# Optimization experiments

Measured on AMD Instinct MI355X. Metric: run time of the kernel, lower is better.

## Reference

```python
import jax, jax.numpy as jnp
import numpy as np

B, S, HID = 2, 2048, 2048
NH, HD = 16, 128            # num heads, head dim (HID = NH*HD)
ROT = 64                    # rotary_dim
MASK_VALUE = -10000.0


def _rotate_every_two(x):
    # x: [..., d] with d even; interleaved (-x2, x1)
    x1 = x[..., ::2]
    x2 = x[..., 1::2]
    return jnp.stack((-x2, x1), axis=-1).reshape(x.shape)


def _fixed_sincos(seq_len, dim):
    inv_freq = 1.0 / (10000.0 ** (jnp.arange(0, dim, 2, dtype=jnp.float32) / dim))
    t = jnp.arange(seq_len, dtype=jnp.float32)
    ang = t[:, None] * inv_freq[None, :]          # [S, dim/2]
    return jnp.sin(ang), jnp.cos(ang)


def _apply_rope(x, sin, cos):
    # x: [B, S, H, rot]; sin/cos: [S, rot/2] -> repeat_interleave(2) -> [S, rot]
    sin = jnp.repeat(sin, 2, axis=-1)[None, :, None, :]
    cos = jnp.repeat(cos, 2, axis=-1)[None, :, None, :]
    return x * cos + _rotate_every_two(x) * sin


def setup_inputs() -> dict:
    key = jax.random.key(0)
    ks = jax.random.split(key, 7)
    w_scale = 1.0 / np.sqrt(HID)
    return {
        "hidden_states": jax.random.normal(ks[0], (B, S, HID), dtype=jnp.float32),
        "attention_mask": jnp.zeros((B, 1, 1, S), dtype=jnp.float32),
        "Wq": jax.random.normal(ks[1], (HID, HID), dtype=jnp.float32) * w_scale,
        "bq": jnp.zeros((HID,), dtype=jnp.float32),
        "Wk": jax.random.normal(ks[2], (HID, HID), dtype=jnp.float32) * w_scale,
        "bk": jnp.zeros((HID,), dtype=jnp.float32),
        "Wv": jax.random.normal(ks[3], (HID, HID), dtype=jnp.float32) * w_scale,
        "bv": jnp.zeros((HID,), dtype=jnp.float32),
    }


def reference(hidden_states, attention_mask, Wq, bq, Wk, bk, Wv, bv):
    # QKV projections (torch Linear: x @ W.T + b)
    q = (hidden_states @ Wq.T + bq).reshape(B, S, NH, HD)
    k = (hidden_states @ Wk.T + bk).reshape(B, S, NH, HD)
    v = (hidden_states @ Wv.T + bv).reshape(B, S, NH, HD)

    # Inline rotary on first ROT dims of q/k
    sin, cos = _fixed_sincos(S, ROT)
    q = jnp.concatenate([_apply_rope(q[..., :ROT], sin, cos), q[..., ROT:]], axis=-1)
    k = jnp.concatenate([_apply_rope(k[..., :ROT], sin, cos), k[..., ROT:]], axis=-1)

    # Scores [B, H, S, S]
    scores = jnp.einsum('bqhd,bkhd->bhqk', q, k) / np.sqrt(HD)

    # Causal mask + additive attention mask
    causal = jnp.tril(jnp.ones((S, S), dtype=bool))[None, None]
    scores = jnp.where(causal, scores, jnp.asarray(MASK_VALUE, scores.dtype))
    scores = scores + attention_mask

    probs = jax.nn.softmax(scores, axis=-1)
    ctx = jnp.einsum('bhqk,bkhd->bqhd', probs, v)
    return ctx.reshape(B, S, HID)
```

## Files before the change

### kernel.cpp

```cpp
#include <hip/hip_runtime.h>

typedef unsigned short bhalf;
typedef __attribute__((ext_vector_type(4))) float    f32x4;
typedef __attribute__((ext_vector_type(8))) short    s16x8;
typedef __attribute__((ext_vector_type(4))) float    floatx4;
typedef __attribute__((ext_vector_type(4))) unsigned int u32x4;
typedef __attribute__((ext_vector_type(4))) unsigned short u16x4;

#define B_  2
#define S_  2048
#define HID_ 2048
#define NH_ 16
#define HD_ 128
#define M_  (B_*S_)
#define MASKV (-10000.0f)

__device__ __forceinline__ bhalf f32_to_bf16(float f) {
    union { float f; unsigned int u; } v; v.f = f;
    unsigned int r = v.u + 0x7FFFu + ((v.u >> 16) & 1u);
    return (bhalf)(r >> 16);
}
__device__ __forceinline__ bhalf f32_to_bf16_trunc(float f) {
    union { float f; unsigned int u; } v; v.f = f;
    return (bhalf)(v.u >> 16);
}
__device__ __forceinline__ float bf16_to_f32(bhalf h) {
    union { unsigned int u; float f; } v; v.u = ((unsigned int)h) << 16;
    return v.f;
}

__device__ __forceinline__ void gl_lds16(const void* g, void* l) {
    __builtin_amdgcn_global_load_lds(
        (const __attribute__((address_space(1))) void*)g,
        (__attribute__((address_space(3))) void*)l, 16, 0, 0);
}

__global__ __launch_bounds__(256) void cast_all(const float* __restrict__ hs,
                                                const float* __restrict__ Wq,
                                                const float* __restrict__ Wk,
                                                const float* __restrict__ Wv,
                                                bhalf* __restrict__ dst) {
    int idx = blockIdx.x * 256 + threadIdx.x;
    const float* src;
    if (idx < 2097152)      src = hs + (size_t)idx * 4;
    else if (idx < 3145728) src = Wq + (size_t)(idx - 2097152) * 4;
    else if (idx < 4194304) src = Wk + (size_t)(idx - 3145728) * 4;
    else                    src = Wv + (size_t)(idx - 4194304) * 4;
    floatx4 f = *(const floatx4*)src;
    u16x4 o;
    o.x = f32_to_bf16(f.x); o.y = f32_to_bf16(f.y);
    o.z = f32_to_bf16(f.z); o.w = f32_to_bf16(f.w);
    *(u16x4*)(dst + (size_t)idx * 4) = o;
}

__global__ __launch_bounds__(256) void qkv_gemm(const bhalf* __restrict__ A,
                                                const bhalf* __restrict__ Wb,
                                                const float* __restrict__ bq,
                                                const float* __restrict__ bk,
                                                const float* __restrict__ bv,
                                                bhalf* __restrict__ Out,
                                                bhalf* __restrict__ VTo) {
    __shared__ __align__(16) bhalf As[128 * 32];
    __shared__ __align__(16) bhalf Bs[128 * 32];
    const int tid  = threadIdx.x;
    const int lane = tid & 63, w = tid >> 6;
    const int wy = w >> 1, wx = w & 1;
    const int quad = lane >> 4, l = lane & 15;
    const int m0 = blockIdx.x * 128, n0 = blockIdx.y * 128;
    const int z  = blockIdx.z;
    const bhalf* W    = Wb + (size_t)z * HID_ * HID_;
    const float* bias = (z == 0) ? bq : (z == 1) ? bk : bv;
    bhalf* out        = Out + (size_t)z * M_ * HID_;

    f32x4 acc[4][4] = {};

    for (int kt = 0; kt < HID_; kt += 32) {
#pragma unroll
        for (int j = 0; j < 2; ++j) {
            int slot0 = j * 256 + w * 64;
            int slot  = slot0 + lane;
            int row = slot >> 2;
            int cg  = (slot & 3) ^ ((row >> 1) & 3);
            gl_lds16(A + (size_t)(m0 + row) * HID_ + kt + cg * 8, As + slot0 * 8);
            gl_lds16(W + (size_t)(n0 + row) * HID_ + kt + cg * 8, Bs + slot0 * 8);
        }
        __syncthreads();
        s16x8 af[4], bfr[4];
#pragma unroll
        for (int mt = 0; mt < 4; ++mt) {
            int row = wy * 64 + mt * 16 + l;
            int cgs = quad ^ ((row >> 1) & 3);
            af[mt] = *(const s16x8*)(As + (row * 4 + cgs) * 8);
        }
#pragma unroll
        for (int nt = 0; nt < 4; ++nt) {
            int row = wx * 64 + nt * 16 + l;
            int cgs = quad ^ ((row >> 1) & 3);
            bfr[nt] = *(const s16x8*)(Bs + (row * 4 + cgs) * 8);
        }
#pragma unroll
        for (int mt = 0; mt < 4; ++mt)
#pragma unroll
            for (int nt = 0; nt < 4; ++nt)
                acc[mt][nt] = __builtin_amdgcn_mfma_f32_16x16x32_bf16(
                    af[mt], bfr[nt], acc[mt][nt], 0, 0, 0);
        __syncthreads();
    }
    if (z == 2) {
#pragma unroll
        for (int mt = 0; mt < 4; ++mt) {
#pragma unroll
            for (int nt = 0; nt < 4; ++nt) {
                int col = n0 + wx * 64 + nt * 16 + l;
                float bv_ = bias[col];
                int row0 = m0 + wy * 64 + mt * 16 + quad * 4;
                int bb = row0 >> 11, s0 = row0 & 2047;
                u16x4 o;
#pragma unroll
                for (int r = 0; r < 4; ++r) o[r] = f32_to_bf16(acc[mt][nt][r] + bv_);
                *(u16x4*)(VTo + ((size_t)(bb * 16) * 128 + col) * S_ + s0) = o;
            }
        }
    } else {
#pragma unroll
        for (int mt = 0; mt < 4; ++mt) {
#pragma unroll
            for (int nt = 0; nt < 4; ++nt) {
                int col = n0 + wx * 64 + nt * 16 + l;
                float bv_ = bias[col];
#pragma unroll
                for (int r = 0; r < 4; ++r) {
                    int row = m0 + wy * 64 + mt * 16 + quad * 4 + r;
                    out[(size_t)row * HID_ + col] = f32_to_bf16(acc[mt][nt][r] + bv_);
                }
            }
        }
    }
}

__global__ __launch_bounds__(256) void rope_table(float2* __restrict__ tab) {
    int idx = blockIdx.x * 256 + threadIdx.x;
    int i = idx & 31, s = idx >> 5;
    float inv = expf(-(float)i * 0.2878231366242557f);
    float ang = (float)s * inv;
    tab[idx] = make_float2(sinf(ang), cosf(ang));
}

__global__ __launch_bounds__(256) void rope_apply(bhalf* __restrict__ Qb,
                                                  bhalf* __restrict__ Kb,
                                                  const float2* __restrict__ tab) {
    int flat = blockIdx.x * 256 + threadIdx.x;
    int i = flat & 31;
    int h = (flat >> 5) & 15;
    int s = (flat >> 9) & 2047;
    int b = flat >> 20;
    size_t base = ((size_t)(b * S_ + s)) * HID_ + h * HD_ + 2 * i;
    float2 sc = tab[s * 32 + i];
    float c = sc.y, sn = sc.x;
    {
        unsigned int q = *(const unsigned int*)(Qb + base);
        float x0 = bf16_to_f32((bhalf)(q & 0xffff));
        float x1 = bf16_to_f32((bhalf)(q >> 16));
        unsigned int o = (unsigned int)f32_to_bf16(x0 * c - x1 * sn)
                       | ((unsigned int)f32_to_bf16(x1 * c + x0 * sn) << 16);
        *(unsigned int*)(Qb + base) = o;
    }
    {
        unsigned int k = *(const unsigned int*)(Kb + base);
        float x0 = bf16_to_f32((bhalf)(k & 0xffff));
        float x1 = bf16_to_f32((bhalf)(k >> 16));
        unsigned int o = (unsigned int)f32_to_bf16(x0 * c - x1 * sn)
                       | ((unsigned int)f32_to_bf16(x1 * c + x0 * sn) << 16);
        *(unsigned int*)(Kb + base) = o;
    }
}

__global__ __launch_bounds__(512, 2) void flash_attn(const bhalf* __restrict__ Qb,
                                                     const bhalf* __restrict__ Kb,
                                                     const bhalf* __restrict__ VT,
                                                     const float* __restrict__ amask,
                                                     float* __restrict__ out) {
    __shared__ __align__(16) bhalf Kbuf[2][2048 * 8];
    __shared__ __align__(16) bhalf Vbuf[2][2048 * 8];
    const int tid = threadIdx.x, lane = tid & 63, w = tid >> 6;
    const int quad = lane >> 4, l = lane & 15;
    const int qt = blockIdx.x, bh = blockIdx.y;
    const int b = bh >> 4, h = bh & 15;
    const bool is_hi = (w < 4);
    const int ws = w & 3;
    const int myrow = is_hi ? ((31 - qt) * 64 + ws * 16) : (qt * 64 + ws * 16);
    const int ch_hi   = (33 - qt) >> 1;
    const int lo_last = (qt * 64 + 63) >> 7;
    const int my_last = is_hi ? (ch_hi - 1) : lo_last;

    s16x8 qf[4];
    {
        const bhalf* Qrow = Qb + (size_t)(b * S_ + myrow + l) * HID_ + h * HD_;
#pragma unroll
        for (int ks = 0; ks < 4; ++ks)
            qf[ks] = *(const s16x8*)(Qrow + ks * 32 + quad * 8);
    }
    s16x8 ones;
#pragma unroll
    for (int j = 0; j < 8; ++j) ones[j] = (short)0x3F80;

    float m_run[4] = {-1e30f, -1e30f, -1e30f, -1e30f};
    f32x4 l_acc = {};
    f32x4 acc[8] = {};
    const int fpl = ((l >> 2) << 1) | (l & 1);

#pragma unroll
    for (int j = 0; j < 4; ++j) {
        int slot0 = j * 512 + w * 64;
        int slot  = slot0 + lane;
        int row = slot >> 4, x = slot & 15;
        int g   = (x & 8) | ((x ^ row) & 7);
        gl_lds16(Kb + (size_t)(b * S_ + row) * HID_ + h * HD_ + g * 8,
                 &Kbuf[0][slot0 * 8]);
        gl_lds16(VT + ((size_t)bh * HD_ + row) * S_ + g * 8,
                 &Vbuf[0][slot0 * 8]);
    }

    for (int kc = 0; kc < ch_hi; ++kc) {
        const int cur = kc & 1, nxt = cur ^ 1;
        const int key0 = kc * 128;
        __syncthreads();

        const bool active = (kc <= my_last);
        const bool diag   = (kc == my_last);

        float am[8];
        if (active) {
#pragma unroll
            for (int nt = 0; nt < 8; ++nt) am[nt] = amask[b * S_ + key0 + nt * 16 + l];
        }
        if (kc + 1 < ch_hi) {
            const int key1 = key0 + 128;
#pragma unroll
            for (int j = 0; j < 4; ++j) {
                int slot0 = j * 512 + w * 64;
                int slot  = slot0 + lane;
                int row = slot >> 4, x = slot & 15;
                int g   = (x & 8) | ((x ^ row) & 7);
                gl_lds16(Kb + (size_t)(b * S_ + key1 + row) * HID_ + h * HD_ + g * 8,
                         &Kbuf[nxt][slot0 * 8]);
                gl_lds16(VT + ((size_t)bh * HD_ + row) * S_ + key1 + g * 8,
                         &Vbuf[nxt][slot0 * 8]);
            }
        }

        const bhalf* Kc = &Kbuf[cur][0];
        const bhalf* Vc = &Vbuf[cur][0];
        bhalf* Pw = &Kbuf[cur][0] + w * 2048;

        f32x4 s[8] = {};
        if (active) {
#pragma unroll
            for (int nt = 0; nt < 8; ++nt) {
                int key = nt * 16 + l;
#pragma unroll
                for (int ks = 0; ks < 4; ++ks) {
                    int dg = ks * 4 + quad;
                    int x  = (dg & 8) | ((dg ^ key) & 7);
                    s16x8 kf = *(const s16x8*)(Kc + (key * 16 + x) * 8);
                    s[nt] = __builtin_amdgcn_mfma_f32_16x16x32_bf16(qf[ks], kf, s[nt], 0, 0, 0);
                }
            }
        }
        __asm__ __volatile__("s_waitcnt lgkmcnt(0)\n\ts_barrier" ::: "memory");

        if (active) {
#pragma unroll
            for (int r = 0; r < 4; ++r) {
                const int qrow = myrow + quad * 4 + r;
                float p[8];
#pragma unroll
                for (int nt = 0; nt < 8; ++nt) {
                    float v = s[nt][r] * 0.08838834764831845f;
                    if (diag) { int key = key0 + nt * 16 + l; v = (key > qrow) ? MASKV : v; }
                    p[nt] = v + am[nt];
                }
                float mx = fmaxf(fmaxf(fmaxf(p[0], p[1]), fmaxf(p[2], p[3])),
                                 fmaxf(fmaxf(p[4], p[5]), fmaxf(p[6], p[7])));
#pragma unroll
                for (int msk = 1; msk < 16; msk <<= 1) mx = fmaxf(mx, __shfl_xor(mx, msk, 64));
                float m_new = fmaxf(m_run[r], mx);
                float alpha = __expf(m_run[r] - m_new);
                m_run[r] = m_new;
                const int m  = quad * 4 + r;
                const int fm = (quad << 1) | (r & 1);
#pragma unroll
                for (int nt = 0; nt < 8; ++nt) {
                    float e = __expf(p[nt] - m_new);
                    int key = nt * 16 + l;
                    Pw[(m * 16 + ((key >> 3) ^ fm)) * 8 + (key & 7)] = f32_to_bf16_trunc(e);
                }
                l_acc[r] *= alpha;
#pragma unroll
                for (int nt = 0; nt < 8; ++nt) acc[nt][r] *= alpha;
            }
#pragma unroll
            for (int kstep = 0; kstep < 4; ++kstep) {
                int kg = kstep * 4 + quad;
                s16x8 pf = *(const s16x8*)(Pw + (l * 16 + (kg ^ fpl)) * 8);
                l_acc = __builtin_amdgcn_mfma_f32_16x16x32_bf16(pf, ones, l_acc, 0, 0, 0);
#pragma unroll
                for (int nt = 0; nt < 8; ++nt) {
                    int d = nt * 16 + l;
                    int x = (kg & 8) | ((kg ^ d) & 7);
                    s16x8 vf = *(const s16x8*)(Vc + (d * 16 + x) * 8);
                    acc[nt] = __builtin_amdgcn_mfma_f32_16x16x32_bf16(pf, vf, acc[nt], 0, 0, 0);
                }
            }
        }
    }

    float inv[4];
#pragma unroll
    for (int r = 0; r < 4; ++r) inv[r] = 1.f / l_acc[r];
#pragma unroll
    for (int nt = 0; nt < 8; ++nt) {
        int col = h * HD_ + nt * 16 + l;
#pragma unroll
        for (int r = 0; r < 4; ++r)
            out[(size_t)(b * S_ + myrow + quad * 4 + r) * HID_ + col] = acc[nt][r] * inv[r];
    }
}

extern "C" void kernel_launch(void* const* d_in, const int* in_sizes, int n_in,
                              void* d_out, int out_size, void* d_ws, size_t ws_size,
                              hipStream_t stream) {
    const float* hs    = (const float*)d_in[0];
    const float* amask = (const float*)d_in[1];
    const float* Wq    = (const float*)d_in[2];
    const float* bq    = (const float*)d_in[3];
    const float* Wk    = (const float*)d_in[4];
    const float* bk    = (const float*)d_in[5];
    const float* Wv    = (const float*)d_in[6];
    const float* bv    = (const float*)d_in[7];
    float* out = (float*)d_out;

    bhalf* hsb = (bhalf*)d_ws;
    bhalf* wqb = hsb + 8388608;
    bhalf* wkb = wqb + 4194304;
    bhalf* wvb = wkb + 4194304;
    bhalf* Qb  = wvb + 4194304;
    bhalf* Kb  = Qb + 8388608;
    bhalf* VTb = Kb + 8388608;
    float2* tab = (float2*)(VTb + 8388608);

    rope_table<<<256, 256, 0, stream>>>(tab);
    cast_all<<<20480, 256, 0, stream>>>(hs, Wq, Wk, Wv, hsb);
    qkv_gemm<<<dim3(32, 16, 3), 256, 0, stream>>>(hsb, wqb, bq, bk, bv, Qb, VTb);
    rope_apply<<<8192, 256, 0, stream>>>(Qb, Kb, tab);
    flash_attn<<<dim3(16, 32), 512, 0, stream>>>(Qb, Kb, VTb, amask, out);
}
```

Measured before the change: 374.8 us.

## Rewrite QKV GEMM with 256x256 tiles, double-buffered LDS and interleaved prefetch

The QKV projection GEMM moves from 128x128 tiles with single-buffered 32-wide K steps to 256x256 tiles on 512 threads, with 64-wide K steps and double-buffered LDS. Global-to-LDS loads for the next K tiles are issued in chunks between MFMA phases, with explicit vmcnt waits, barriers and setprio raised around the MFMA blocks. The aim is to increase data reuse per tile and hide memory latency behind matrix math. The cost is higher register and LDS use per block (128KB LDS, launch bounds of 2 blocks) and only 384 blocks in the grid, so GPU occupancy and fill may drop.

```diff
diff --git a/kernel.cpp b/kernel.cpp
--- a/kernel.cpp
+++ b/kernel.cpp
@@ -4,7 +4,6 @@
 typedef __attribute__((ext_vector_type(4))) float    f32x4;
 typedef __attribute__((ext_vector_type(8))) short    s16x8;
 typedef __attribute__((ext_vector_type(4))) float    floatx4;
-typedef __attribute__((ext_vector_type(4))) unsigned int u32x4;
 typedef __attribute__((ext_vector_type(4))) unsigned short u16x4;
 
 #define B_  2
@@ -33,6 +32,12 @@
     __builtin_amdgcn_global_load_lds(
         (const __attribute__((address_space(1))) void*)g,
         (__attribute__((address_space(3))) void*)l, 16, 0, 0);
+}
+
+__device__ __forceinline__ void pb() {
+    __builtin_amdgcn_sched_barrier(0);
+    __builtin_amdgcn_s_barrier();
+    __builtin_amdgcn_sched_barrier(0);
 }
 
 __global__ __launch_bounds__(256) void cast_all(const float* __restrict__ hs,
@@ -53,67 +58,142 @@
     *(u16x4*)(dst + (size_t)idx * 4) = o;
 }
 
-__global__ __launch_bounds__(256) void qkv_gemm(const bhalf* __restrict__ A,
-                                                const bhalf* __restrict__ Wb,
-                                                const float* __restrict__ bq,
-                                                const float* __restrict__ bk,
-                                                const float* __restrict__ bv,
-                                                bhalf* __restrict__ Out,
-                                                bhalf* __restrict__ VTo) {
-    __shared__ __align__(16) bhalf As[128 * 32];
-    __shared__ __align__(16) bhalf Bs[128 * 32];
+__global__ __launch_bounds__(512, 2) void qkv_gemm(const bhalf* __restrict__ A,
+                                                   const bhalf* __restrict__ Wb,
+                                                   const float* __restrict__ bq,
+                                                   const float* __restrict__ bk,
+                                                   const float* __restrict__ bv,
+                                                   bhalf* __restrict__ Out,
+                                                   bhalf* __restrict__ VTo) {
+    __shared__ __align__(16) bhalf As[2][16384];
+    __shared__ __align__(16) bhalf Bs[2][16384];
     const int tid  = threadIdx.x;
     const int lane = tid & 63, w = tid >> 6;
-    const int wy = w >> 1, wx = w & 1;
     const int quad = lane >> 4, l = lane & 15;
-    const int m0 = blockIdx.x * 128, n0 = blockIdx.y * 128;
+    const int wy = w >> 2, wx = w & 3;
+    const int m0 = blockIdx.x * 256, n0 = blockIdx.y * 256;
     const int z  = blockIdx.z;
     const bhalf* W    = Wb + (size_t)z * HID_ * HID_;
     const float* bias = (z == 0) ? bq : (z == 1) ? bk : bv;
     bhalf* out        = Out + (size_t)z * M_ * HID_;
 
-    f32x4 acc[4][4] = {};
-
-    for (int kt = 0; kt < HID_; kt += 32) {
-#pragma unroll
-        for (int j = 0; j < 2; ++j) {
-            int slot0 = j * 256 + w * 64;
-            int slot  = slot0 + lane;
-            int row = slot >> 2;
-            int cg  = (slot & 3) ^ ((row >> 1) & 3);
-            gl_lds16(A + (size_t)(m0 + row) * HID_ + kt + cg * 8, As + slot0 * 8);
-            gl_lds16(W + (size_t)(n0 + row) * HID_ + kt + cg * 8, Bs + slot0 * 8);
-        }
-        __syncthreads();
-        s16x8 af[4], bfr[4];
-#pragma unroll
-        for (int mt = 0; mt < 4; ++mt) {
-            int row = wy * 64 + mt * 16 + l;
-            int cgs = quad ^ ((row >> 1) & 3);
-            af[mt] = *(const s16x8*)(As + (row * 4 + cgs) * 8);
-        }
-#pragma unroll
-        for (int nt = 0; nt < 4; ++nt) {
-            int row = wx * 64 + nt * 16 + l;
-            int cgs = quad ^ ((row >> 1) & 3);
-            bfr[nt] = *(const s16x8*)(Bs + (row * 4 + cgs) * 8);
-        }
-#pragma unroll
-        for (int mt = 0; mt < 4; ++mt)
-#pragma unroll
-            for (int nt = 0; nt < 4; ++nt)
-                acc[mt][nt] = __builtin_amdgcn_mfma_f32_16x16x32_bf16(
-                    af[mt], bfr[nt], acc[mt][nt], 0, 0, 0);
-        __syncthreads();
-    }
+    const int row_s = tid >> 3;
+    const int kg_s  = (tid & 7) ^ (row_s & 7);
+
+#define SA(bf, t, u) gl_lds16(A + (size_t)(m0 + (u)*64 + row_s) * HID_ + (t)*64 + kg_s*8, \
+                              &As[bf][(u)*4096 + w*512])
+#define SB(bf, t, u) gl_lds16(W + (size_t)(n0 + (u)*64 + row_s) * HID_ + (t)*64 + kg_s*8, \
+                              &Bs[bf][(u)*4096 + w*512])
+#define FRAG(P, row, ks) (*(const s16x8*)((P) + (row)*64 + ((((ks)*4 + quad) ^ ((row)&7)) * 8)))
+
+    f32x4 acc[8][4] = {};
+
+    SA(0, 0, 0); SA(0, 0, 2);
+    SB(0, 0, 0); SB(0, 0, 1); SB(0, 0, 2); SB(0, 0, 3);
+    SA(0, 0, 1); SA(0, 0, 3);
+    SA(1, 1, 0); SA(1, 1, 2);
+    SB(1, 1, 0); SB(1, 1, 1); SB(1, 1, 2); SB(1, 1, 3);
+    asm volatile("s_waitcnt vmcnt(6)" ::: "memory");
+    pb();
+
+    for (int t = 0; t < 32; ++t) {
+        const int cur = t & 1, nxt = cur ^ 1;
+        const bhalf* Ac = &As[cur][0];
+        const bhalf* Bc = &Bs[cur][0];
+        const int arow = wy * 128 + l;
+        const int brow = wx * 64 + l;
+        s16x8 a[4][2], b01[2][2], b23[2][2];
+
+#pragma unroll
+        for (int mt = 0; mt < 4; ++mt)
+#pragma unroll
+            for (int ks = 0; ks < 2; ++ks)
+                a[mt][ks] = FRAG(Ac, arow + mt * 16, ks);
+#pragma unroll
+        for (int nt = 0; nt < 2; ++nt)
+#pragma unroll
+            for (int ks = 0; ks < 2; ++ks)
+                b01[nt][ks] = FRAG(Bc, brow + nt * 16, ks);
+        if (t + 1 < 32) { SA(nxt, t + 1, 1); SA(nxt, t + 1, 3); }
+        pb();
+        __builtin_amdgcn_s_setprio(1);
+#pragma unroll
+        for (int mt = 0; mt < 4; ++mt)
+#pragma unroll
+            for (int nt = 0; nt < 2; ++nt)
+#pragma unroll
+                for (int ks = 0; ks < 2; ++ks)
+                    acc[mt][nt] = __builtin_amdgcn_mfma_f32_16x16x32_bf16(
+                        a[mt][ks], b01[nt][ks], acc[mt][nt], 0, 0, 0);
+        __builtin_amdgcn_s_setprio(0);
+        pb();
+
+#pragma unroll
+        for (int nt = 0; nt < 2; ++nt)
+#pragma unroll
+            for (int ks = 0; ks < 2; ++ks)
+                b23[nt][ks] = FRAG(Bc, brow + (nt + 2) * 16, ks);
+        if (t + 2 < 32) { SA(cur, t + 2, 0); SA(cur, t + 2, 2); }
+        pb();
+        __builtin_amdgcn_s_setprio(1);
+#pragma unroll
+        for (int mt = 0; mt < 4; ++mt)
+#pragma unroll
+            for (int nt = 0; nt < 2; ++nt)
+#pragma unroll
+                for (int ks = 0; ks < 2; ++ks)
+                    acc[mt][nt + 2] = __builtin_amdgcn_mfma_f32_16x16x32_bf16(
+                        a[mt][ks], b23[nt][ks], acc[mt][nt + 2], 0, 0, 0);
+        __builtin_amdgcn_s_setprio(0);
+        pb();
+
+#pragma unroll
+        for (int mt = 0; mt < 4; ++mt)
+#pragma unroll
+            for (int ks = 0; ks < 2; ++ks)
+                a[mt][ks] = FRAG(Ac, arow + 64 + mt * 16, ks);
+        if (t + 2 < 32) { SB(cur, t + 2, 0); SB(cur, t + 2, 1); }
+        pb();
+        __builtin_amdgcn_s_setprio(1);
+#pragma unroll
+        for (int mt = 0; mt < 4; ++mt)
+#pragma unroll
+            for (int nt = 0; nt < 2; ++nt)
+#pragma unroll
+                for (int ks = 0; ks < 2; ++ks)
+                    acc[4 + mt][nt + 2] = __builtin_amdgcn_mfma_f32_16x16x32_bf16(
+                        a[mt][ks], b23[nt][ks], acc[4 + mt][nt + 2], 0, 0, 0);
+        __builtin_amdgcn_s_setprio(0);
+        pb();
+
+        if (t + 2 < 32) { SB(cur, t + 2, 2); SB(cur, t + 2, 3); }
+        if (t < 30) { asm volatile("s_waitcnt vmcnt(6)" ::: "memory"); }
+        else        { asm volatile("s_waitcnt vmcnt(0)" ::: "memory"); }
+        pb();
+        __builtin_amdgcn_s_setprio(1);
+#pragma unroll
+        for (int mt = 0; mt < 4; ++mt)
+#pragma unroll
+            for (int nt = 0; nt < 2; ++nt)
+#pragma unroll
+                for (int ks = 0; ks < 2; ++ks)
+                    acc[4 + mt][nt] = __builtin_amdgcn_mfma_f32_16x16x32_bf16(
+                        a[mt][ks], b01[nt][ks], acc[4 + mt][nt], 0, 0, 0);
+        __builtin_amdgcn_s_setprio(0);
+        pb();
+    }
+#undef SA
+#undef SB
+#undef FRAG
+
     if (z == 2) {
 #pragma unroll
-        for (int mt = 0; mt < 4; ++mt) {
+        for (int mt = 0; mt < 8; ++mt) {
 #pragma unroll
             for (int nt = 0; nt < 4; ++nt) {
                 int col = n0 + wx * 64 + nt * 16 + l;
                 float bv_ = bias[col];
-                int row0 = m0 + wy * 64 + mt * 16 + quad * 4;
+                int row0 = m0 + wy * 128 + mt * 16 + quad * 4;
                 int bb = row0 >> 11, s0 = row0 & 2047;
                 u16x4 o;
 #pragma unroll
@@ -123,14 +203,14 @@
         }
     } else {
 #pragma unroll
-        for (int mt = 0; mt < 4; ++mt) {
+        for (int mt = 0; mt < 8; ++mt) {
 #pragma unroll
             for (int nt = 0; nt < 4; ++nt) {
                 int col = n0 + wx * 64 + nt * 16 + l;
                 float bv_ = bias[col];
 #pragma unroll
                 for (int r = 0; r < 4; ++r) {
-                    int row = m0 + wy * 64 + mt * 16 + quad * 4 + r;
+                    int row = m0 + wy * 128 + mt * 16 + quad * 4 + r;
                     out[(size_t)row * HID_ + col] = f32_to_bf16(acc[mt][nt][r] + bv_);
                 }
             }
@@ -351,7 +431,7 @@
 
     rope_table<<<256, 256, 0, stream>>>(tab);
     cast_all<<<20480, 256, 0, stream>>>(hs, Wq, Wk, Wv, hsb);
-    qkv_gemm<<<dim3(32, 16, 3), 256, 0, stream>>>(hsb, wqb, bq, bk, bv, Qb, VTb);
+    qkv_gemm<<<dim3(16, 8, 3), 512, 0, stream>>>(hsb, wqb, bq, bk, bv, Qb, VTb);
     rope_apply<<<8192, 256, 0, stream>>>(Qb, Kb, tab);
     flash_attn<<<dim3(16, 32), 512, 0, stream>>>(Qb, Kb, VTb, amask, out);
 }
```

After: 377.5 us. Within noise of the previous version (+0.7%).

## Rewrite QKV GEMM with 256x256 tiles, BK=64, and double-buffered LDS pipeline

Applied to the files above, without the earlier changes.

Replaces the 128x128 single-buffered QKV GEMM with 256x256 tiles over 512 threads and a 64-wide K step. The LDS buffers are double-buffered and global-to-LDS loads are interleaved with MFMA phases using explicit s_barrier, vmcnt waits and setprio. The goal is to raise arithmetic intensity and hide global load latency behind matrix math. It uses 128 KB of LDS and more accumulator registers per thread, and the grid shrinks to 384 blocks, which may leave some compute units underused.

```diff
diff --git a/kernel.cpp b/kernel.cpp
--- a/kernel.cpp
+++ b/kernel.cpp
@@ -4,7 +4,6 @@
 typedef __attribute__((ext_vector_type(4))) float    f32x4;
 typedef __attribute__((ext_vector_type(8))) short    s16x8;
 typedef __attribute__((ext_vector_type(4))) float    floatx4;
-typedef __attribute__((ext_vector_type(4))) unsigned int u32x4;
 typedef __attribute__((ext_vector_type(4))) unsigned short u16x4;
 
 #define B_  2
@@ -34,6 +33,8 @@
         (const __attribute__((address_space(1))) void*)g,
         (__attribute__((address_space(3))) void*)l, 16, 0, 0);
 }
+
+#define BARRIER() asm volatile("s_barrier" ::: "memory")
 
 __global__ __launch_bounds__(256) void cast_all(const float* __restrict__ hs,
                                                 const float* __restrict__ Wq,
@@ -53,67 +54,153 @@
     *(u16x4*)(dst + (size_t)idx * 4) = o;
 }
 
-__global__ __launch_bounds__(256) void qkv_gemm(const bhalf* __restrict__ A,
-                                                const bhalf* __restrict__ Wb,
-                                                const float* __restrict__ bq,
-                                                const float* __restrict__ bk,
-                                                const float* __restrict__ bv,
-                                                bhalf* __restrict__ Out,
-                                                bhalf* __restrict__ VTo) {
-    __shared__ __align__(16) bhalf As[128 * 32];
-    __shared__ __align__(16) bhalf Bs[128 * 32];
+__global__ __launch_bounds__(512, 2) void qkv_gemm(const bhalf* __restrict__ A,
+                                                   const bhalf* __restrict__ Wb,
+                                                   const float* __restrict__ bq,
+                                                   const float* __restrict__ bk,
+                                                   const float* __restrict__ bv,
+                                                   bhalf* __restrict__ Out,
+                                                   bhalf* __restrict__ VTo) {
+    __shared__ __align__(16) bhalf As[2][16384];
+    __shared__ __align__(16) bhalf Bs[2][16384];
     const int tid  = threadIdx.x;
     const int lane = tid & 63, w = tid >> 6;
-    const int wy = w >> 1, wx = w & 1;
     const int quad = lane >> 4, l = lane & 15;
-    const int m0 = blockIdx.x * 128, n0 = blockIdx.y * 128;
+    const int wy = w >> 2, wx = w & 3;
+    const int m0 = blockIdx.x * 256, n0 = blockIdx.y * 256;
     const int z  = blockIdx.z;
     const bhalf* W    = Wb + (size_t)z * HID_ * HID_;
     const float* bias = (z == 0) ? bq : (z == 1) ? bk : bv;
     bhalf* out        = Out + (size_t)z * M_ * HID_;
 
-    f32x4 acc[4][4] = {};
-
-    for (int kt = 0; kt < HID_; kt += 32) {
-#pragma unroll
-        for (int j = 0; j < 2; ++j) {
-            int slot0 = j * 256 + w * 64;
-            int slot  = slot0 + lane;
-            int row = slot >> 2;
-            int cg  = (slot & 3) ^ ((row >> 1) & 3);
-            gl_lds16(A + (size_t)(m0 + row) * HID_ + kt + cg * 8, As + slot0 * 8);
-            gl_lds16(W + (size_t)(n0 + row) * HID_ + kt + cg * 8, Bs + slot0 * 8);
-        }
-        __syncthreads();
-        s16x8 af[4], bfr[4];
-#pragma unroll
-        for (int mt = 0; mt < 4; ++mt) {
-            int row = wy * 64 + mt * 16 + l;
-            int cgs = quad ^ ((row >> 1) & 3);
-            af[mt] = *(const s16x8*)(As + (row * 4 + cgs) * 8);
-        }
-#pragma unroll
-        for (int nt = 0; nt < 4; ++nt) {
-            int row = wx * 64 + nt * 16 + l;
-            int cgs = quad ^ ((row >> 1) & 3);
-            bfr[nt] = *(const s16x8*)(Bs + (row * 4 + cgs) * 8);
-        }
-#pragma unroll
-        for (int mt = 0; mt < 4; ++mt)
-#pragma unroll
-            for (int nt = 0; nt < 4; ++nt)
-                acc[mt][nt] = __builtin_amdgcn_mfma_f32_16x16x32_bf16(
-                    af[mt], bfr[nt], acc[mt][nt], 0, 0, 0);
-        __syncthreads();
-    }
+    bhalf* AsF = &As[0][0];
+    bhalf* BsF = &Bs[0][0];
+
+    const int row_s = tid >> 3;
+    const int kg_s  = (tid & 7) ^ (row_s & 7);
+    const int w512  = w * 512;
+
+    const bhalf* gA0 = A + (size_t)(m0 +   0 + row_s) * HID_ + kg_s * 8;
+    const bhalf* gA1 = A + (size_t)(m0 +  64 + row_s) * HID_ + kg_s * 8;
+    const bhalf* gA2 = A + (size_t)(m0 + 128 + row_s) * HID_ + kg_s * 8;
+    const bhalf* gA3 = A + (size_t)(m0 + 192 + row_s) * HID_ + kg_s * 8;
+    const bhalf* gB0 = W + (size_t)(n0 +   0 + row_s) * HID_ + kg_s * 8;
+    const bhalf* gB1 = W + (size_t)(n0 +  64 + row_s) * HID_ + kg_s * 8;
+    const bhalf* gB2 = W + (size_t)(n0 + 128 + row_s) * HID_ + kg_s * 8;
+    const bhalf* gB3 = W + (size_t)(n0 + 192 + row_s) * HID_ + kg_s * 8;
+
+    const int aIdx = (wy * 128 + l) * 64;
+    const int bIdx = (wx * 64  + l) * 64;
+    const int swz0 = ((0 + quad) ^ (l & 7)) * 8;
+    const int swz1 = ((4 + quad) ^ (l & 7)) * 8;
+
+    f32x4 acc[8][4] = {};
+
+#define ADV() do { gA0 += 64; gA1 += 64; gA2 += 64; gA3 += 64;               \
+                   gB0 += 64; gB1 += 64; gB2 += 64; gB3 += 64; } while (0)
+
+#define KTILE(BUF, ST1, ST2, VM) do {                                        \
+    const int CB = (BUF) * 16384, NB = ((BUF) ^ 1) * 16384;                  \
+    s16x8 a_[4][2], b01_[2][2], b23_[2][2];                                  \
+                    \
+    _Pragma("unroll") for (int mt = 0; mt < 4; ++mt) {                       \
+        a_[mt][0] = *(const s16x8*)(AsF + CB + aIdx + mt * 1024 + swz0);     \
+        a_[mt][1] = *(const s16x8*)(AsF + CB + aIdx + mt * 1024 + swz1); }   \
+    _Pragma("unroll") for (int nt = 0; nt < 2; ++nt) {                       \
+        b01_[nt][0] = *(const s16x8*)(BsF + CB + bIdx + nt * 1024 + swz0);   \
+        b01_[nt][1] = *(const s16x8*)(BsF + CB + bIdx + nt * 1024 + swz1); } \
+    if (ST1) { gl_lds16(gA1 + 64, AsF + NB + 1 * 4096 + w512);               \
+               gl_lds16(gA3 + 64, AsF + NB + 3 * 4096 + w512); }             \
+    BARRIER();                                                               \
+    __builtin_amdgcn_s_setprio(1);                                           \
+    _Pragma("unroll") for (int mt = 0; mt < 4; ++mt)                         \
+      _Pragma("unroll") for (int nt = 0; nt < 2; ++nt)                       \
+        _Pragma("unroll") for (int ks = 0; ks < 2; ++ks)                     \
+          acc[mt][nt] = __builtin_amdgcn_mfma_f32_16x16x32_bf16(             \
+              a_[mt][ks], b01_[nt][ks], acc[mt][nt], 0, 0, 0);               \
+    __builtin_amdgcn_s_setprio(0);                                           \
+    BARRIER();                                                               \
+                           \
+    _Pragma("unroll") for (int nt = 0; nt < 2; ++nt) {                       \
+        b23_[nt][0] = *(const s16x8*)(BsF + CB + bIdx + (nt+2)*1024 + swz0); \
+        b23_[nt][1] = *(const s16x8*)(BsF + CB + bIdx + (nt+2)*1024 + swz1);}\
+    if (ST2) { gl_lds16(gA0 + 128, AsF + CB + 0 * 4096 + w512);              \
+               gl_lds16(gA2 + 128, AsF + CB + 2 * 4096 + w512); }            \
+    BARRIER();                                                               \
+    __builtin_amdgcn_s_setprio(1);                                           \
+    _Pragma("unroll") for (int mt = 0; mt < 4; ++mt)                         \
+      _Pragma("unroll") for (int nt = 0; nt < 2; ++nt)                       \
+        _Pragma("unroll") for (int ks = 0; ks < 2; ++ks)                     \
+          acc[mt][nt + 2] = __builtin_amdgcn_mfma_f32_16x16x32_bf16(         \
+              a_[mt][ks], b23_[nt][ks], acc[mt][nt + 2], 0, 0, 0);           \
+    __builtin_amdgcn_s_setprio(0);                                           \
+    BARRIER();                                                               \
+                        \
+    _Pragma("unroll") for (int mt = 0; mt < 4; ++mt) {                       \
+        a_[mt][0] = *(const s16x8*)(AsF + CB + aIdx + 4096 + mt*1024 + swz0);\
+        a_[mt][1] = *(const s16x8*)(AsF + CB + aIdx + 4096 + mt*1024 + swz1);}\
+    if (ST2) { gl_lds16(gB0 + 128, BsF + CB + 0 * 4096 + w512);              \
+               gl_lds16(gB1 + 128, BsF + CB + 1 * 4096 + w512); }            \
+    BARRIER();                                                               \
+    __builtin_amdgcn_s_setprio(1);                                           \
+    _Pragma("unroll") for (int mt = 0; mt < 4; ++mt)                         \
+      _Pragma("unroll") for (int nt = 0; nt < 2; ++nt)                       \
+        _Pragma("unroll") for (int ks = 0; ks < 2; ++ks)                     \
+          acc[4 + mt][nt + 2] = __builtin_amdgcn_mfma_f32_16x16x32_bf16(     \
+              a_[mt][ks], b23_[nt][ks], acc[4 + mt][nt + 2], 0, 0, 0);       \
+    __builtin_amdgcn_s_setprio(0);                                           \
+    BARRIER();                                                               \
+    \
+    if (ST2) { gl_lds16(gB2 + 128, BsF + CB + 2 * 4096 + w512);              \
+               gl_lds16(gB3 + 128, BsF + CB + 3 * 4096 + w512); }            \
+    if ((VM) == 6)      asm volatile("s_waitcnt vmcnt(6)" ::: "memory");     \
+    else if ((VM) == 0) asm volatile("s_waitcnt vmcnt(0)" ::: "memory");     \
+    BARRIER();                                                               \
+    __builtin_amdgcn_s_setprio(1);                                           \
+    _Pragma("unroll") for (int mt = 0; mt < 4; ++mt)                         \
+      _Pragma("unroll") for (int nt = 0; nt < 2; ++nt)                       \
+        _Pragma("unroll") for (int ks = 0; ks < 2; ++ks)                     \
+          acc[4 + mt][nt] = __builtin_amdgcn_mfma_f32_16x16x32_bf16(         \
+              a_[mt][ks], b01_[nt][ks], acc[4 + mt][nt], 0, 0, 0);           \
+    __builtin_amdgcn_s_setprio(0);                                           \
+    BARRIER();                                                               \
+} while (0)
+
+    gl_lds16(gA0, AsF + 0 * 4096 + w512);
+    gl_lds16(gA2, AsF + 2 * 4096 + w512);
+    gl_lds16(gB0, BsF + 0 * 4096 + w512);
+    gl_lds16(gB1, BsF + 1 * 4096 + w512);
+    gl_lds16(gB2, BsF + 2 * 4096 + w512);
+    gl_lds16(gB3, BsF + 3 * 4096 + w512);
+    gl_lds16(gA1, AsF + 1 * 4096 + w512);
+    gl_lds16(gA3, AsF + 3 * 4096 + w512);
+    gl_lds16(gA0 + 64, AsF + 16384 + 0 * 4096 + w512);
+    gl_lds16(gA2 + 64, AsF + 16384 + 2 * 4096 + w512);
+    gl_lds16(gB0 + 64, BsF + 16384 + 0 * 4096 + w512);
+    gl_lds16(gB1 + 64, BsF + 16384 + 1 * 4096 + w512);
+    gl_lds16(gB2 + 64, BsF + 16384 + 2 * 4096 + w512);
+    gl_lds16(gB3 + 64, BsF + 16384 + 3 * 4096 + w512);
+    asm volatile("s_waitcnt vmcnt(6)" ::: "memory");
+    BARRIER();
+
+    for (int tt = 0; tt < 15; ++tt) {
+        KTILE(0, 1, 1, 6); ADV();
+        KTILE(1, 1, 1, 6); ADV();
+    }
+    KTILE(0, 1, 0, 0); ADV();
+    KTILE(1, 0, 0, -1);
+
+#undef KTILE
+#undef ADV
+
     if (z == 2) {
 #pragma unroll
-        for (int mt = 0; mt < 4; ++mt) {
+        for (int mt = 0; mt < 8; ++mt) {
 #pragma unroll
             for (int nt = 0; nt < 4; ++nt) {
                 int col = n0 + wx * 64 + nt * 16 + l;
                 float bv_ = bias[col];
-                int row0 = m0 + wy * 64 + mt * 16 + quad * 4;
+                int row0 = m0 + wy * 128 + mt * 16 + quad * 4;
                 int bb = row0 >> 11, s0 = row0 & 2047;
                 u16x4 o;
 #pragma unroll
@@ -123,14 +210,14 @@
         }
     } else {
 #pragma unroll
-        for (int mt = 0; mt < 4; ++mt) {
+        for (int mt = 0; mt < 8; ++mt) {
 #pragma unroll
             for (int nt = 0; nt < 4; ++nt) {
                 int col = n0 + wx * 64 + nt * 16 + l;
                 float bv_ = bias[col];
 #pragma unroll
                 for (int r = 0; r < 4; ++r) {
-                    int row = m0 + wy * 64 + mt * 16 + quad * 4 + r;
+                    int row = m0 + wy * 128 + mt * 16 + quad * 4 + r;
                     out[(size_t)row * HID_ + col] = f32_to_bf16(acc[mt][nt][r] + bv_);
                 }
             }
@@ -351,7 +438,7 @@
 
     rope_table<<<256, 256, 0, stream>>>(tab);
     cast_all<<<20480, 256, 0, stream>>>(hs, Wq, Wk, Wv, hsb);
-    qkv_gemm<<<dim3(32, 16, 3), 256, 0, stream>>>(hsb, wqb, bq, bk, bv, Qb, VTb);
+    qkv_gemm<<<dim3(16, 8, 3), 512, 0, stream>>>(hsb, wqb, bq, bk, bv, Qb, VTb);
     rope_apply<<<8192, 256, 0, stream>>>(Qb, Kb, tab);
     flash_attn<<<dim3(16, 32), 512, 0, stream>>>(Qb, Kb, VTb, amask, out);
 }
```

After: 361.9 us. -3.5%, faster.
